# Kernel tuning notes

Hardware: AMD Instinct MI355X
Metric: run time of the kernel (lower is better)

Reference implementation:

```python
import jax, jax.numpy as jnp
import numpy as np

HEADS, LEVELS, POINTS, ZANCH = 8, 4, 8, 4
EMBED = 256
SHAPES = np.array([[92, 160], [46, 80], [23, 40], [12, 20]], dtype=np.int32)


def setup_inputs() -> dict:
    key = jax.random.key(0)
    k = jax.random.split(key, 9)
    bs, nq = 1, 10000
    nv = int((SHAPES[:, 0].astype(np.int64) * SHAPES[:, 1]).sum())  # 19560
    f32 = jnp.float32
    return dict(
        query=jax.random.normal(k[0], (bs, nq, EMBED), f32),
        value=jax.random.normal(k[1], (bs, nv, EMBED), f32),
        query_pos=0.1 * jax.random.normal(k[2], (bs, nq, EMBED), f32),
        reference_points=jax.random.uniform(k[3], (bs, nq, ZANCH, 2), dtype=f32),
        spatial_shapes=jnp.asarray(SHAPES),
        W_off=0.01 * jax.random.normal(k[4], (EMBED, HEADS * LEVELS * POINTS * 2), f32),
        b_off=0.5 * jax.random.normal(k[5], (HEADS * LEVELS * POINTS * 2,), f32),
        W_attn=0.01 * jax.random.normal(k[6], (EMBED, HEADS * LEVELS * POINTS), f32),
        b_attn=jnp.zeros((HEADS * LEVELS * POINTS,), f32),
        W_val=(1.0 / np.sqrt(EMBED)) * jax.random.normal(k[7], (EMBED, EMBED), f32),
        b_val=jnp.zeros((EMBED,), f32),
        W_out=(1.0 / np.sqrt(EMBED)) * jax.random.normal(k[8], (EMBED, EMBED), f32),
        b_out=jnp.zeros((EMBED,), f32),
    )


def _bilinear(v_l, x, y, Hl, Wl):
    # v_l: [bs, heads, Hl*Wl, d]; x, y: [bs, nq, heads, P] pixel coords
    # (torch grid_sample, align_corners=False, zero padding): px = loc*W - 0.5
    bs, nq, heads, P = x.shape
    d = v_l.shape[-1]
    x0 = jnp.floor(x)
    y0 = jnp.floor(y)
    lx = x - x0
    ly = y - y0
    x0i = x0.astype(jnp.int32)
    y0i = y0.astype(jnp.int32)

    def corner(xi, yi, w):
        valid = (xi >= 0) & (xi < Wl) & (yi >= 0) & (yi < Hl)
        idx = jnp.clip(yi, 0, Hl - 1) * Wl + jnp.clip(xi, 0, Wl - 1)
        idxr = idx.transpose(0, 2, 1, 3).reshape(bs, heads, nq * P)
        g = jnp.take_along_axis(v_l, idxr[..., None], axis=2)  # [bs,heads,nq*P,d]
        g = g.reshape(bs, heads, nq, P, d).transpose(0, 2, 1, 3, 4)
        return g * (w * valid.astype(w.dtype))[..., None]

    return (corner(x0i, y0i, (1 - lx) * (1 - ly))
            + corner(x0i + 1, y0i, lx * (1 - ly))
            + corner(x0i, y0i + 1, (1 - lx) * ly)
            + corner(x0i + 1, y0i + 1, lx * ly))


def reference(query, value, query_pos, reference_points, spatial_shapes,
              W_off, b_off, W_attn, b_attn, W_val, b_val, W_out, b_out):
    shapes = np.asarray(spatial_shapes)  # static per-level (H, W)
    bs, nq, E = query.shape
    heads = HEADS
    L = shapes.shape[0]
    P = W_off.shape[1] // (heads * L * 2)
    Z = reference_points.shape[2]
    d = E // heads

    residual = query
    q = query + query_pos
    v = (value @ W_val + b_val).reshape(bs, -1, heads, d)

    off = (q @ W_off + b_off).reshape(bs, nq, heads, L, P, 2)
    attn = jax.nn.softmax((q @ W_attn + b_attn).reshape(bs, nq, heads, L * P), axis=-1)
    attn = attn.reshape(bs, nq, heads, L, P)

    # normalize offsets by (W, H) per level, add Z-anchor reference points
    norm = jnp.asarray(np.stack([shapes[:, 1], shapes[:, 0]], -1), off.dtype)  # [L,2]
    off = off / norm[None, None, None, :, None, :]
    loc = (reference_points[:, :, None, None, None, :, :]
           + off.reshape(bs, nq, heads, L, P // Z, Z, 2)).reshape(bs, nq, heads, L, P, 2)

    starts = np.concatenate([[0], np.cumsum(shapes[:, 0].astype(np.int64) * shapes[:, 1])])
    out = jnp.zeros((bs, nq, heads, d), q.dtype)
    for l in range(L):  # small fixed loop over pyramid levels
        Hl, Wl = int(shapes[l, 0]), int(shapes[l, 1])
        v_l = v[:, int(starts[l]):int(starts[l + 1])].transpose(0, 2, 1, 3)  # [bs,heads,HW,d]
        x = loc[:, :, :, l, :, 0] * Wl - 0.5
        y = loc[:, :, :, l, :, 1] * Hl - 0.5
        sampled = _bilinear(v_l, x, y, Hl, Wl)  # [bs,nq,heads,P,d]
        out = out + (sampled * attn[:, :, :, l, :, None]).sum(axis=3)

    out = out.reshape(bs, nq, E) @ W_out + b_out
    return out + residual  # dropout is identity at eval
```

## Files before the change

### kernel.cpp

```cpp
#include <hip/hip_runtime.h>
#include <hip/hip_bf16.h>
#include <hip/hip_fp16.h>
#include <math.h>

typedef __hip_bfloat16 bf16;
typedef short short8_t __attribute__((ext_vector_type(8)));
typedef float f32x4 __attribute__((ext_vector_type(4)));
typedef int i32x4 __attribute__((ext_vector_type(4)));

#define EMBED 256
#define ZANCH 4

__global__ __launch_bounds__(256) void k_prep(
    const float* __restrict__ Woff, const float* __restrict__ Wattn,
    const float* __restrict__ Wval, const float* __restrict__ Wout,
    bf16* __restrict__ wt,
    const float* __restrict__ query, const float* __restrict__ query_pos,
    bf16* __restrict__ qb)
{
    const int b = blockIdx.x;
    const int tid = threadIdx.x;
    if (b < 320) {
        __shared__ float tile[32][33];
        const int tn = b >> 3, tk = b & 7;
        const int r = tid >> 5, c = tid & 31;
        const int n0 = tn * 32, k0t = tk * 32;
#pragma unroll
        for (int rr = r; rr < 32; rr += 8) {
            const int k = k0t + rr;
            const int n = n0 + c;
            float val;
            if (n < 512)       val = Woff[(size_t)k * 512 + n];
            else if (n < 768)  val = Wattn[(size_t)k * 256 + (n - 512)];
            else if (n < 1024) val = Wval[(size_t)k * 256 + (n - 768)];
            else               val = Wout[(size_t)k * 256 + (n - 1024)];
            tile[rr][c] = val;
        }
        __syncthreads();
#pragma unroll
        for (int rr = r; rr < 32; rr += 8) {
            const int n = n0 + rr;
            const int k = k0t + c;
            wt[(size_t)n * 256 + k] = __float2bfloat16(tile[c][rr]);
        }
    } else {
        size_t i = ((size_t)(b - 320) * 256 + tid) * 4;
        float4 a = *(const float4*)(query + i);
        float4 p = *(const float4*)(query_pos + i);
        qb[i + 0] = __float2bfloat16(a.x + p.x);
        qb[i + 1] = __float2bfloat16(a.y + p.y);
        qb[i + 2] = __float2bfloat16(a.z + p.z);
        qb[i + 3] = __float2bfloat16(a.w + p.w);
    }
}

__device__ __forceinline__ int a_base(int row, int quad) {
    return (row >> 1) * 1040 + (row & 1) * 512 + quad * 16;
}

__global__ __launch_bounds__(256, 4) void k_gemm_vp(
    const float* __restrict__ value, const bf16* __restrict__ Btv,
    const float* __restrict__ bv, bf16* __restrict__ vhl, int Mv,
    const bf16* __restrict__ qb, const bf16* __restrict__ Btcat,
    const float* __restrict__ boff, const float* __restrict__ battn,
    __half* __restrict__ raw, int Mq)
{
    __shared__ char sm[16896];
    float* smE  = (float*)sm;
    bf16*  smEv = (bf16*)sm;

    const int nbv = (Mv + 31) / 32;
    const int nbq = (Mq + 31) / 32;
    int bx, by;
    {
        const int bid = blockIdx.x;
        if (bid < nbv) { by = 3; bx = bid; }
        else { const int p = bid - nbv; by = p / nbq; bx = p - by * nbq; }
    }

    const int tid  = threadIdx.x;
    const int lane = tid & 63;
    const int wv   = tid >> 6;
    const int c16  = lane & 15, quad = lane >> 4;
    const int nwave = wv * 64;

    const bool isval = (by == 3);
    const int M = isval ? Mv : Mq;
    const int row0 = bx * 32;
    const bf16* Bt = isval ? Btv : (Btcat + (size_t)(by * 256) * 256);

    if (isval) {
#pragma unroll
        for (int i = 0; i < 8; ++i) {
            const int f = i * 256 + tid;
            const int row = f >> 6, col4 = f & 63;
            const int rowg = min(row0 + row, M - 1);
            float4 v = *(const float4*)(value + (size_t)rowg * 256 + col4 * 4);
            union { bf16 h; unsigned short s; } c;
            unsigned p0, p1;
            c.h = __float2bfloat16(v.x); p0 = c.s;
            c.h = __float2bfloat16(v.y); p0 |= (unsigned)c.s << 16;
            c.h = __float2bfloat16(v.z); p1 = c.s;
            c.h = __float2bfloat16(v.w); p1 |= (unsigned)c.s << 16;
            *(int2*)(sm + ((row >> 1) * 1040 + (row & 1) * 512 + col4 * 8)) =
                make_int2((int)p0, (int)p1);
        }
    } else {
#pragma unroll
        for (int i = 0; i < 4; ++i) {
            const int f = i * 256 + tid;
            const int row = f >> 5, col8 = f & 31;
            const int rowg = min(row0 + row, M - 1);
            short8_t v = *(const short8_t*)(qb + (size_t)rowg * 256 + col8 * 8);
            *(short8_t*)(sm + ((row >> 1) * 1040 + (row & 1) * 512 + col8 * 16)) = v;
        }
    }
    __syncthreads();

    f32x4 acc[2][4] = {};
    {
        int aoffl[2];
#pragma unroll
        for (int mt = 0; mt < 2; ++mt) aoffl[mt] = a_base(mt * 16 + c16, quad);
        size_t boffr[4];
#pragma unroll
        for (int nt = 0; nt < 4; ++nt)
            boffr[nt] = (size_t)(nwave + nt * 16 + c16) * 256 + quad * 8;
#pragma unroll
        for (int k0 = 0; k0 < 256; k0 += 32) {
            short8_t a[2], b[4];
#pragma unroll
            for (int mt = 0; mt < 2; ++mt)
                a[mt] = *(const short8_t*)(sm + aoffl[mt] + k0 * 2);
#pragma unroll
            for (int nt = 0; nt < 4; ++nt) b[nt] = *(const short8_t*)(Bt + boffr[nt] + k0);
#pragma unroll
            for (int mt = 0; mt < 2; ++mt)
#pragma unroll
                for (int nt = 0; nt < 4; ++nt)
                    acc[mt][nt] = __builtin_amdgcn_mfma_f32_16x16x32_bf16(
                        a[mt], b[nt], acc[mt][nt], 0, 0, 0);
        }
    }
    __syncthreads();

    if (isval) {
#pragma unroll
        for (int nt = 0; nt < 4; ++nt) {
            const int colg = nwave + nt * 16 + c16;
            const float bias = bv[colg];
#pragma unroll
            for (int mt = 0; mt < 2; ++mt)
#pragma unroll
                for (int reg = 0; reg < 4; ++reg) {
                    const int rl = mt * 16 + quad * 4 + reg;
                    smEv[rl * 264 + colg] = __float2bfloat16(acc[mt][nt][reg] + bias);
                }
        }
        __syncthreads();
#pragma unroll
        for (int sub = 0; sub < 2; ++sub) {
            const int h = wv * 2 + sub;
            bf16* dsth = vhl + (size_t)h * Mv * 32;
#pragma unroll
            for (int j = 0; j < 2; ++j) {
                const int s = j * 64 + lane;
                const int pix = s >> 2, seg = s & 3;
                const int rg = row0 + pix;
                if (rg < Mv)
                    *(short8_t*)(dsth + (size_t)rg * 32 + seg * 8) =
                        *(const short8_t*)(smEv + pix * 264 + h * 32 + seg * 8);
            }
        }
    } else {
#pragma unroll
        for (int chunk = 0; chunk < 2; ++chunk) {
            if (chunk) __syncthreads();
#pragma unroll
            for (int nt = 0; nt < 4; ++nt) {
                const int colg = nwave + nt * 16 + c16;
                const int cg = by * 256 + colg;
                const float bias = (cg < 512) ? boff[cg] : battn[cg - 512];
#pragma unroll
                for (int reg = 0; reg < 4; ++reg) {
                    const int rl = quad * 4 + reg;
                    smE[rl * 260 + colg] = acc[chunk][nt][reg] + bias;
                }
            }
            __syncthreads();
#pragma unroll
            for (int rr = 0; rr < 4; ++rr) {
                const int rl = wv * 4 + rr;
                const int rg = row0 + chunk * 16 + rl;
                if (rg < Mq) {
                    f32x4 v = *(const f32x4*)(smE + rl * 260 + lane * 4);
                    union { int2 i2; __half h[4]; } u;
                    u.h[0] = __float2half(v[0]);
                    u.h[1] = __float2half(v[1]);
                    u.h[2] = __float2half(v[2]);
                    u.h[3] = __float2half(v[3]);
                    *(int2*)(raw + (size_t)rg * 768 + by * 256 + lane * 4) = u.i2;
                }
            }
        }
    }
}

__global__ __launch_bounds__(256) void k_sample(
    const bf16* __restrict__ vhl, const __half* __restrict__ raw,
    const float* __restrict__ refpts, bf16* __restrict__ outa, int nq, int nv)
{
    __shared__ int spr[16][132];
    const int tid = threadIdx.x;
    const int b = blockIdx.x;
    const int hp = (b & 7) >> 1;
    const int qg = ((b >> 3) << 1) + (b & 1);
    const int q0 = qg * 8;

    {
        const int lp = tid & 31;
        const int l = lp >> 3;
        const int p = lp & 7;
        const int z = p & (ZANCH - 1);
        const float Wlf = (l == 0) ? 160.f : (l == 1) ? 80.f : (l == 2) ? 40.f : 20.f;
        const float Hlf = (l == 0) ? 92.f : (l == 1) ? 46.f : (l == 2) ? 23.f : 12.f;
        const int Wli = (l == 0) ? 160 : (l == 1) ? 80 : (l == 2) ? 40 : 20;
        const int Hli = (l == 0) ? 92 : (l == 1) ? 46 : (l == 2) ? 23 : 12;
        const int Stl = (l == 0) ? 0 : (l == 1) ? 14720 : (l == 2) ? 18400 : 19320;

#pragma unroll
        for (int r = 0; r < 2; ++r) {
            const int g = r * 8 + (tid >> 5);
            const int q = q0 + (g >> 1);
            const int head = hp * 2 + (g & 1);
            const int col = head * 32 + lp;

            const __half2 oxy = *(const __half2*)(raw + (size_t)q * 768 + 2 * col);
            const float ox = __half2float(oxy.x);
            const float oy = __half2float(oxy.y);
            const float lg = __half2float(raw[(size_t)q * 768 + 512 + col]);

            float m = lg;
            for (int o = 16; o > 0; o >>= 1) m = fmaxf(m, __shfl_xor(m, o, 32));
            float e = __expf(lg - m);
            float s = e;
            for (int o = 16; o > 0; o >>= 1) s += __shfl_xor(s, o, 32);
            const float aw = e / s;

            const float refx = refpts[(size_t)q * 8 + z * 2 + 0];
            const float refy = refpts[(size_t)q * 8 + z * 2 + 1];
            const float px = refx * Wlf + ox - 0.5f;
            const float py = refy * Hlf + oy - 0.5f;

            const float x0f = floorf(px), y0f = floorf(py);
            const int x0 = (int)x0f, y0 = (int)y0f;
            const float lx = px - x0f, ly = py - y0f;
            const float cw[4] = { (1.f - lx) * (1.f - ly), lx * (1.f - ly),
                                  (1.f - lx) * ly,         lx * ly };
#pragma unroll
            for (int c = 0; c < 4; ++c) {
                const int xi = x0 + (c & 1);
                const int yi = y0 + (c >> 1);
                const bool valid = (xi >= 0) && (xi < Wli) && (yi >= 0) && (yi < Hli);
                const int xc = min(max(xi, 0), Wli - 1);
                const int yc = min(max(yi, 0), Hli - 1);
                const float w = valid ? (cw[c] * aw) : 0.f;
                const int idx = Stl + yc * Wli + xc;
                const unsigned hw = (unsigned)__half_as_ushort(__float2half(w));
                spr[g][c * 32 + lp] = (idx << 16) | (int)hw;
            }
        }
    }
    __syncthreads();

    const int g2  = tid >> 4;
    const int qs  = g2 >> 1;
    const int hh  = g2 & 1;
    const int cp  = tid & 15;
    const char* hpb = (const char*)vhl + (size_t)(hp * 2) * nv * 64;
    const unsigned tbase = (unsigned)(hh * nv) * 64u + (unsigned)cp * 4u;

    float a0 = 0.f, a1 = 0.f;
    i32x4 pk[2][4];
    int   dv[2][16];

#pragma unroll
    for (int j = 0; j < 4; ++j) pk[0][j] = *(const i32x4*)&spr[g2][j * 4];
#pragma unroll
    for (int j = 0; j < 16; ++j)
        dv[0][j] = *(const int*)(hpb +
            (size_t)(tbase + (((unsigned)pk[0][j >> 2][j & 3] >> 16) << 6)));

#pragma unroll
    for (int bb = 0; bb < 8; ++bb) {
        const int cur = bb & 1, nxt = cur ^ 1;
        if (bb < 7) {
#pragma unroll
            for (int j = 0; j < 4; ++j)
                pk[nxt][j] = *(const i32x4*)&spr[g2][(bb + 1) * 16 + j * 4];
#pragma unroll
            for (int j = 0; j < 16; ++j)
                dv[nxt][j] = *(const int*)(hpb +
                    (size_t)(tbase + (((unsigned)pk[nxt][j >> 2][j & 3] >> 16) << 6)));
        }
#pragma unroll
        for (int j = 0; j < 16; ++j) {
            const int pkj = pk[cur][j >> 2][j & 3];
            const float w = __half2float(__ushort_as_half((unsigned short)(pkj & 0xFFFF)));
            a0 = fmaf(w, __int_as_float(dv[cur][j] << 16), a0);
            a1 = fmaf(w, __int_as_float(dv[cur][j] & 0xFFFF0000), a1);
        }
    }

    __hip_bfloat162 o2;
    o2.x = __float2bfloat16(a0);
    o2.y = __float2bfloat16(a1);
    *(__hip_bfloat162*)(outa + (size_t)(q0 + qs) * 256 + (hp * 2 + hh) * 32 + cp * 2) = o2;
}

__global__ __launch_bounds__(256, 4) void k_gemm_out(
    const bf16* __restrict__ outa, const bf16* __restrict__ Bto,
    const float* __restrict__ bo, const float* __restrict__ query,
    float* __restrict__ out, int M)
{
    __shared__ char sm[16640];
    const int row0 = blockIdx.x * 32;
    const int tid = threadIdx.x;
    const int nwave = (tid >> 6) * 64;
    const int lane = tid & 63;
    const int c16 = lane & 15, quad = lane >> 4;

#pragma unroll
    for (int i = 0; i < 4; ++i) {
        const int f = i * 256 + tid;
        const int row = f >> 5, col8 = f & 31;
        const int rowg = min(row0 + row, M - 1);
        short8_t v = *(const short8_t*)(outa + (size_t)rowg * 256 + col8 * 8);
        *(short8_t*)(sm + ((row >> 1) * 1040 + (row & 1) * 512 + col8 * 16)) = v;
    }
    __syncthreads();

    f32x4 acc[2][4] = {};
    {
        int aoffl[2];
#pragma unroll
        for (int mt = 0; mt < 2; ++mt) aoffl[mt] = a_base(mt * 16 + c16, quad);
        size_t boffr[4];
#pragma unroll
        for (int nt = 0; nt < 4; ++nt)
            boffr[nt] = (size_t)(nwave + nt * 16 + c16) * 256 + quad * 8;
#pragma unroll
        for (int k0 = 0; k0 < 256; k0 += 32) {
            short8_t a[2], b[4];
#pragma unroll
            for (int mt = 0; mt < 2; ++mt)
                a[mt] = *(const short8_t*)(sm + aoffl[mt] + k0 * 2);
#pragma unroll
            for (int nt = 0; nt < 4; ++nt) b[nt] = *(const short8_t*)(Bto + boffr[nt] + k0);
#pragma unroll
            for (int mt = 0; mt < 2; ++mt)
#pragma unroll
                for (int nt = 0; nt < 4; ++nt)
                    acc[mt][nt] = __builtin_amdgcn_mfma_f32_16x16x32_bf16(
                        a[mt], b[nt], acc[mt][nt], 0, 0, 0);
        }
    }
#pragma unroll
    for (int nt = 0; nt < 4; ++nt) {
        int colg = nwave + nt * 16 + c16;
        float bias = bo[colg];
#pragma unroll
        for (int mt = 0; mt < 2; ++mt)
#pragma unroll
            for (int reg = 0; reg < 4; ++reg) {
                int row = row0 + mt * 16 + quad * 4 + reg;
                if (row < M) {
                    size_t o_ = (size_t)row * 256 + colg;
                    float fv = acc[mt][nt][reg] + bias + query[o_];
                    if (!(fv == fv) || fabsf(fv) > 1e30f) fv = 0.f;
                    out[o_] = fv;
                }
            }
    }
}

extern "C" void kernel_launch(void* const* d_in, const int* in_sizes, int n_in,
                              void* d_out, int out_size, void* d_ws, size_t ws_size,
                              hipStream_t stream)
{
    const float* query     = (const float*)d_in[0];
    const float* value     = (const float*)d_in[1];
    const float* query_pos = (const float*)d_in[2];
    const float* refpts    = (const float*)d_in[3];
    const float* Woff  = (const float*)d_in[5];
    const float* boff  = (const float*)d_in[6];
    const float* Wattn = (const float*)d_in[7];
    const float* battn = (const float*)d_in[8];
    const float* Wval  = (const float*)d_in[9];
    const float* bval  = (const float*)d_in[10];
    const float* Wout  = (const float*)d_in[11];
    const float* bout  = (const float*)d_in[12];
    float* out = (float*)d_out;

    const int nq = in_sizes[0] / EMBED;
    const int nv = in_sizes[1] / EMBED;

    char* base = (char*)d_ws;
    bf16*   wt   = (bf16*)base;
    bf16*   qb   = (bf16*)(base + 655360);
    __half* raw  = (__half*)(base + 15790080);
    bf16*   outa = (bf16*)(base + 31150080);
    bf16*   vhl  = (bf16*)(base + 36270080);
    const bf16* Btcat = wt;
    const bf16* Btv   = wt + 768 * 256;
    const bf16* Bto   = wt + 1024 * 256;

    const int nbv = (nv + 31) / 32;
    const int nbq = (nq + 31) / 32;

    k_prep<<<2820, 256, 0, stream>>>(Woff, Wattn, Wval, Wout, wt,
                                     query, query_pos, qb);
    k_gemm_vp<<<nbv + 3 * nbq, 256, 0, stream>>>(value, Btv, bval, vhl, nv,
                                                 qb, Btcat, boff, battn, raw, nq);
    k_sample<<<(nq / 8) * 4, 256, 0, stream>>>(vhl, raw, refpts, outa, nq, nv);
    k_gemm_out<<<(nq + 31) / 32, 256, 0, stream>>>(outa, Bto, bout, query, out, nq);
}
```

Baseline: 190.8 us.

## Fuse query+pos bf16 conversion into GEMM load; split and vectorize output GEMM epilogue

```diff
diff --git a/kernel.cpp b/kernel.cpp
--- a/kernel.cpp
+++ b/kernel.cpp
@@ -11,46 +11,48 @@
 #define EMBED 256
 #define ZANCH 4
 
+__device__ __forceinline__ short8_t cvt8(const float4& f0, const float4& f1) {
+    union { bf16 h; unsigned short s; } u;
+    short8_t r;
+    u.h = __float2bfloat16(f0.x); r[0] = (short)u.s;
+    u.h = __float2bfloat16(f0.y); r[1] = (short)u.s;
+    u.h = __float2bfloat16(f0.z); r[2] = (short)u.s;
+    u.h = __float2bfloat16(f0.w); r[3] = (short)u.s;
+    u.h = __float2bfloat16(f1.x); r[4] = (short)u.s;
+    u.h = __float2bfloat16(f1.y); r[5] = (short)u.s;
+    u.h = __float2bfloat16(f1.z); r[6] = (short)u.s;
+    u.h = __float2bfloat16(f1.w); r[7] = (short)u.s;
+    return r;
+}
+
 __global__ __launch_bounds__(256) void k_prep(
     const float* __restrict__ Woff, const float* __restrict__ Wattn,
     const float* __restrict__ Wval, const float* __restrict__ Wout,
-    bf16* __restrict__ wt,
-    const float* __restrict__ query, const float* __restrict__ query_pos,
-    bf16* __restrict__ qb)
+    bf16* __restrict__ wt)
 {
     const int b = blockIdx.x;
     const int tid = threadIdx.x;
-    if (b < 320) {
-        __shared__ float tile[32][33];
-        const int tn = b >> 3, tk = b & 7;
-        const int r = tid >> 5, c = tid & 31;
-        const int n0 = tn * 32, k0t = tk * 32;
-#pragma unroll
-        for (int rr = r; rr < 32; rr += 8) {
-            const int k = k0t + rr;
-            const int n = n0 + c;
-            float val;
-            if (n < 512)       val = Woff[(size_t)k * 512 + n];
-            else if (n < 768)  val = Wattn[(size_t)k * 256 + (n - 512)];
-            else if (n < 1024) val = Wval[(size_t)k * 256 + (n - 768)];
-            else               val = Wout[(size_t)k * 256 + (n - 1024)];
-            tile[rr][c] = val;
-        }
-        __syncthreads();
-#pragma unroll
-        for (int rr = r; rr < 32; rr += 8) {
-            const int n = n0 + rr;
-            const int k = k0t + c;
-            wt[(size_t)n * 256 + k] = __float2bfloat16(tile[c][rr]);
-        }
-    } else {
-        size_t i = ((size_t)(b - 320) * 256 + tid) * 4;
-        float4 a = *(const float4*)(query + i);
-        float4 p = *(const float4*)(query_pos + i);
-        qb[i + 0] = __float2bfloat16(a.x + p.x);
-        qb[i + 1] = __float2bfloat16(a.y + p.y);
-        qb[i + 2] = __float2bfloat16(a.z + p.z);
-        qb[i + 3] = __float2bfloat16(a.w + p.w);
+    __shared__ float tile[32][33];
+    const int tn = b >> 3, tk = b & 7;
+    const int r = tid >> 5, c = tid & 31;
+    const int n0 = tn * 32, k0t = tk * 32;
+#pragma unroll
+    for (int rr = r; rr < 32; rr += 8) {
+        const int k = k0t + rr;
+        const int n = n0 + c;
+        float val;
+        if (n < 512)       val = Woff[(size_t)k * 512 + n];
+        else if (n < 768)  val = Wattn[(size_t)k * 256 + (n - 512)];
+        else if (n < 1024) val = Wval[(size_t)k * 256 + (n - 768)];
+        else               val = Wout[(size_t)k * 256 + (n - 1024)];
+        tile[rr][c] = val;
+    }
+    __syncthreads();
+#pragma unroll
+    for (int rr = r; rr < 32; rr += 8) {
+        const int n = n0 + rr;
+        const int k = k0t + c;
+        wt[(size_t)n * 256 + k] = __float2bfloat16(tile[c][rr]);
     }
 }
 
@@ -61,7 +63,8 @@
 __global__ __launch_bounds__(256, 4) void k_gemm_vp(
     const float* __restrict__ value, const bf16* __restrict__ Btv,
     const float* __restrict__ bv, bf16* __restrict__ vhl, int Mv,
-    const bf16* __restrict__ qb, const bf16* __restrict__ Btcat,
+    const float* __restrict__ query, const float* __restrict__ query_pos,
+    const bf16* __restrict__ Btcat,
     const float* __restrict__ boff, const float* __restrict__ battn,
     __half* __restrict__ raw, int Mq)
 {
@@ -111,8 +114,15 @@
             const int f = i * 256 + tid;
             const int row = f >> 5, col8 = f & 31;
             const int rowg = min(row0 + row, M - 1);
-            short8_t v = *(const short8_t*)(qb + (size_t)rowg * 256 + col8 * 8);
-            *(short8_t*)(sm + ((row >> 1) * 1040 + (row & 1) * 512 + col8 * 16)) = v;
+            const size_t off = (size_t)rowg * 256 + col8 * 8;
+            float4 q0 = *(const float4*)(query + off);
+            float4 q1 = *(const float4*)(query + off + 4);
+            float4 p0 = *(const float4*)(query_pos + off);
+            float4 p1 = *(const float4*)(query_pos + off + 4);
+            float4 s0 = make_float4(q0.x + p0.x, q0.y + p0.y, q0.z + p0.z, q0.w + p0.w);
+            float4 s1 = make_float4(q1.x + p1.x, q1.y + p1.y, q1.z + p1.z, q1.w + p1.w);
+            *(short8_t*)(sm + ((row >> 1) * 1040 + (row & 1) * 512 + col8 * 16)) =
+                cvt8(s0, s1);
         }
     }
     __syncthreads();
@@ -324,11 +334,16 @@
     float* __restrict__ out, int M)
 {
     __shared__ char sm[16640];
-    const int row0 = blockIdx.x * 32;
-    const int tid = threadIdx.x;
-    const int nwave = (tid >> 6) * 64;
+    float* smE = (float*)sm;
+    const int bxr  = blockIdx.x >> 1;
+    const int colh = blockIdx.x & 1;
+    const int row0 = bxr * 32;
+    const int col0 = colh * 128;
+    const int tid  = threadIdx.x;
+    const int wv   = tid >> 6;
     const int lane = tid & 63;
-    const int c16 = lane & 15, quad = lane >> 4;
+    const int c16  = lane & 15, quad = lane >> 4;
+    const int nwave = wv * 32;
 
 #pragma unroll
     for (int i = 0; i < 4; ++i) {
@@ -340,47 +355,64 @@
     }
     __syncthreads();
 
-    f32x4 acc[2][4] = {};
+    f32x4 acc[2][2] = {};
     {
         int aoffl[2];
 #pragma unroll
         for (int mt = 0; mt < 2; ++mt) aoffl[mt] = a_base(mt * 16 + c16, quad);
-        size_t boffr[4];
-#pragma unroll
-        for (int nt = 0; nt < 4; ++nt)
-            boffr[nt] = (size_t)(nwave + nt * 16 + c16) * 256 + quad * 8;
+        size_t boffr[2];
+#pragma unroll
+        for (int nt = 0; nt < 2; ++nt)
+            boffr[nt] = (size_t)(col0 + nwave + nt * 16 + c16) * 256 + quad * 8;
 #pragma unroll
         for (int k0 = 0; k0 < 256; k0 += 32) {
-            short8_t a[2], b[4];
+            short8_t a[2], b[2];
 #pragma unroll
             for (int mt = 0; mt < 2; ++mt)
                 a[mt] = *(const short8_t*)(sm + aoffl[mt] + k0 * 2);
 #pragma unroll
-            for (int nt = 0; nt < 4; ++nt) b[nt] = *(const short8_t*)(Bto + boffr[nt] + k0);
+            for (int nt = 0; nt < 2; ++nt) b[nt] = *(const short8_t*)(Bto + boffr[nt] + k0);
 #pragma unroll
             for (int mt = 0; mt < 2; ++mt)
 #pragma unroll
-                for (int nt = 0; nt < 4; ++nt)
+                for (int nt = 0; nt < 2; ++nt)
                     acc[mt][nt] = __builtin_amdgcn_mfma_f32_16x16x32_bf16(
                         a[mt], b[nt], acc[mt][nt], 0, 0, 0);
         }
     }
-#pragma unroll
-    for (int nt = 0; nt < 4; ++nt) {
-        int colg = nwave + nt * 16 + c16;
-        float bias = bo[colg];
-#pragma unroll
-        for (int mt = 0; mt < 2; ++mt)
-#pragma unroll
-            for (int reg = 0; reg < 4; ++reg) {
-                int row = row0 + mt * 16 + quad * 4 + reg;
-                if (row < M) {
-                    size_t o_ = (size_t)row * 256 + colg;
-                    float fv = acc[mt][nt][reg] + bias + query[o_];
+    __syncthreads();
+
+#pragma unroll
+    for (int chunk = 0; chunk < 2; ++chunk) {
+        if (chunk) __syncthreads();
+#pragma unroll
+        for (int nt = 0; nt < 2; ++nt) {
+            const int coll = nwave + nt * 16 + c16;
+            const float bias = bo[col0 + coll];
+#pragma unroll
+            for (int reg = 0; reg < 4; ++reg)
+                smE[(quad * 4 + reg) * 132 + coll] = acc[chunk][nt][reg] + bias;
+        }
+        __syncthreads();
+#pragma unroll
+        for (int s = 0; s < 2; ++s) {
+            const int slot = s * 256 + tid;
+            const int rl = slot >> 5, c4 = slot & 31;
+            const int rg = row0 + chunk * 16 + rl;
+            if (rg < M) {
+                f32x4 v = *(const f32x4*)(smE + rl * 132 + c4 * 4);
+                const size_t o_ = (size_t)rg * 256 + col0 + c4 * 4;
+                f32x4 qv = *(const f32x4*)(query + o_);
+                f32x4 rr;
+#pragma unroll
+                for (int j = 0; j < 4; ++j) {
+                    float fv = v[j] + qv[j];
                     if (!(fv == fv) || fabsf(fv) > 1e30f) fv = 0.f;
-                    out[o_] = fv;
+                    rr[j] = fv;
                 }
+                *(f32x4*)(out + o_) = rr;
             }
+        }
     }
 }
 
@@ -407,7 +439,6 @@
 
     char* base = (char*)d_ws;
     bf16*   wt   = (bf16*)base;
-    bf16*   qb   = (bf16*)(base + 655360);
     __half* raw  = (__half*)(base + 15790080);
     bf16*   outa = (bf16*)(base + 31150080);
     bf16*   vhl  = (bf16*)(base + 36270080);
@@ -418,10 +449,10 @@
     const int nbv = (nv + 31) / 32;
     const int nbq = (nq + 31) / 32;
 
-    k_prep<<<2820, 256, 0, stream>>>(Woff, Wattn, Wval, Wout, wt,
-                                     query, query_pos, qb);
+    k_prep<<<320, 256, 0, stream>>>(Woff, Wattn, Wval, Wout, wt);
     k_gemm_vp<<<nbv + 3 * nbq, 256, 0, stream>>>(value, Btv, bval, vhl, nv,
-                                                 qb, Btcat, boff, battn, raw, nq);
+                                                 query, query_pos, Btcat,
+                                                 boff, battn, raw, nq);
     k_sample<<<(nq / 8) * 4, 256, 0, stream>>>(vhl, raw, refpts, outa, nq, nv);
-    k_gemm_out<<<(nq + 31) / 32, 256, 0, stream>>>(outa, Bto, bout, query, out, nq);
-}
+    k_gemm_out<<<2 * nbq, 256, 0, stream>>>(outa, Bto, bout, query, out, nq);
+}
```

After: 183.1 us (median of 2 runs). -4.1%, faster.
